# Kernel tuning notes

Measured on AMD Instinct MI355X. Metric: run time of the kernel, lower is better.

Reference implementation:

```python
import jax, jax.numpy as jnp
import numpy as np

B, CIN, COUT, K = 8, 16, 32, 3
D = H = W = 64
NUM_W = CIN * COUT * K ** 3  # 13824
NUM_P = NUM_W + COUT         # 13856


def setup_inputs() -> dict:
    key = jax.random.key(0)
    ks = jax.random.split(key, 10)
    stdv = 1.0 / np.sqrt(CIN * K ** 3)
    return {
        "x": jax.random.normal(ks[0], (B, CIN, D, H, W), jnp.float32),
        "features": jax.random.normal(ks[1], (B, 10), jnp.float32),
        "fc0_w": jax.random.normal(ks[2], (16, 10), jnp.float32) * 0.3,
        "fc0_b": jax.random.normal(ks[3], (16,), jnp.float32) * 0.1,
        "a0": jnp.full((1,), 0.25, jnp.float32),
        "fc1_w": jax.random.normal(ks[4], (8, 16), jnp.float32) * 0.25,
        "fc1_b": jax.random.normal(ks[5], (8,), jnp.float32) * 0.1,
        "a1": jnp.full((1,), 0.25, jnp.float32),
        "wg_w": jax.random.uniform(ks[6], (NUM_P, 8), jnp.float32, -stdv, stdv),
        "wg_b": jax.random.uniform(ks[7], (NUM_P,), jnp.float32, -stdv / 100, stdv / 100),
    }


def _prelu(x, a):
    return jnp.where(x >= 0, x, a * x)


def reference(x, features, fc0_w, fc0_b, a0, fc1_w, fc1_b, a1, wg_w, wg_b):
    # hypernet MLP: [B,10] -> [B,16] -> [B,8] -> [B,NUM_P]
    h = _prelu(features @ fc0_w.T + fc0_b, a0)
    h = _prelu(h @ fc1_w.T + fc1_b, a1)
    params = h @ wg_w.T + wg_b  # [B, NUM_P]
    weights = params[:, :NUM_W].reshape(B, COUT, CIN, K, K, K)
    biases = params[:, NUM_W:]  # [B, COUT]

    def conv_one(xi, wi, bi):
        # xi: [CIN,D,H,W], wi: [COUT,CIN,K,K,K], bi: [COUT]
        y = jax.lax.conv_general_dilated(
            xi[None], wi, window_strides=(1, 1, 1),
            padding=[(1, 1)] * 3,
            dimension_numbers=("NCDHW", "OIDHW", "NCDHW"))
        return y[0] + bi[:, None, None, None]

    return jax.vmap(conv_one)(x, weights, biases)  # [B,COUT,D,H,W]
```

## Files before the change

### kernel.cpp

```cpp
#include <hip/hip_runtime.h>

typedef short short8 __attribute__((ext_vector_type(8)));
typedef float floatx4 __attribute__((ext_vector_type(4)));

#define BB   8
#define CIN  16
#define COUT 32
#define DD   64
#define NUM_W (CIN * COUT * 27)
#define NUM_P (NUM_W + COUT)
#define KPAD  448


__device__ __forceinline__ short f2bf(float f) {
    union { float f; unsigned u; } v; v.f = f;
    unsigned r = v.u + 0x7FFF + ((v.u >> 16) & 1);
    return (short)(r >> 16);
}

__device__ __forceinline__ unsigned pack2bf(float lo, float hi) {
    union { float f; unsigned u; } a, b; a.f = lo; b.f = hi;
    unsigned ra = a.u + 0x7FFF + ((a.u >> 16) & 1);
    unsigned rb = b.u + 0x7FFF + ((b.u >> 16) & 1);
    return (ra >> 16) | (rb & 0xFFFF0000u);
}

__device__ __forceinline__ int swz(int byte) {
    return byte ^ (((byte >> 7) & 7) << 4);
}

__global__ void hyper_kernel(const float* __restrict__ features,
                             const float* __restrict__ fc0_w,
                             const float* __restrict__ fc0_b,
                             const float* __restrict__ a0,
                             const float* __restrict__ fc1_w,
                             const float* __restrict__ fc1_b,
                             const float* __restrict__ a1,
                             const float* __restrict__ wg_w,
                             const float* __restrict__ wg_b,
                             float* __restrict__ h1out,
                             float* __restrict__ biasout) {
    __shared__ float h0[8][16];
    __shared__ float h1s[8][8];
    const int t = threadIdx.x;
    if (t < 128) {
        const int b = t >> 4, i = t & 15;
        float s = fc0_b[i];
        #pragma unroll
        for (int j = 0; j < 10; ++j) s += features[b * 10 + j] * fc0_w[i * 10 + j];
        const float a = a0[0];
        h0[b][i] = (s >= 0.f) ? s : a * s;
    }
    __syncthreads();
    if (t < 64) {
        const int b = t >> 3, i = t & 7;
        float s = fc1_b[i];
        #pragma unroll
        for (int j = 0; j < 16; ++j) s += h0[b][j] * fc1_w[i * 16 + j];
        const float a = a1[0];
        const float r = (s >= 0.f) ? s : a * s;
        h1s[b][i] = r;
        h1out[b * 8 + i] = r;
    }
    __syncthreads();
    {
        const int b = t >> 5, co = t & 31;
        const int p = NUM_W + co;
        float s = wg_b[p];
        #pragma unroll
        for (int j = 0; j < 8; ++j) s += h1s[b][j] * wg_w[p * 8 + j];
        biasout[b * 32 + co] = s;
    }
}

__global__ void wgen_kernel(const float* __restrict__ h1,
                            const float* __restrict__ wg_w,
                            const float* __restrict__ wg_b,
                            short* __restrict__ A) {
    const int b  = blockIdx.y;
    const int id = blockIdx.x * 256 + threadIdx.x;
    const int tap  = id % 28;
    const int rest = id / 28;
    const int ci   = rest & 15;
    const int co   = rest >> 4;
    float val = 0.f;
    if (tap < 27) {
        const int p = co * 432 + ci * 27 + tap;
        float s = wg_b[p];
        #pragma unroll
        for (int j = 0; j < 8; ++j) s += h1[b * 8 + j] * wg_w[p * 8 + j];
        val = s;
    }
    A[(b * 32 + co) * KPAD + tap * 16 + ci] = f2bf(val);
}

__global__ __launch_bounds__(256, 2) void conv_mfma_kernel(
        const float* __restrict__ x,
        const short* __restrict__ A,
        const float* __restrict__ bias,
        float* __restrict__ out) {
    __shared__ uint4 xs4[2376];
    __shared__ uint4 als4[1664];
    char* xsb = (char*)xs4;
    char* alb = (char*)als4;

    const int t    = threadIdx.x;
    const int lane = t & 63;
    const int wave = t >> 6;
    const int n16  = lane & 15;
    const int q    = lane >> 4;

    const int lin = (blockIdx.z * 64 + blockIdx.y) * 16 + blockIdx.x;
    const int o   = (lin & 7) * 1024 + (lin >> 3);
    const int h0  = (o & 15) * 4;
    const int d   = (o >> 4) & 63;
    const int b   = o >> 10;

    const short* Ab = A + (size_t)(b * 32) * KPAD;

    #pragma unroll
    for (int i = 0; i < 7; ++i) {
        const int u = t + i * 256;
        if (u < 1664) {
            const int cm = u >> 6;
            const int c  = cm >> 1, mt = cm & 1;
            const int nn = (u >> 2) & 15, qs = u & 3;
            als4[u] = *(const uint4*)(Ab + (mt * 16 + nn) * KPAD + c * 32 + qs * 8);
        }
    }

    short8 af13[2];
    af13[0] = *(const short8*)(Ab + n16 * KPAD + 13 * 32 + q * 8);
    af13[1] = *(const short8*)(Ab + (16 + n16) * KPAD + 13 * 32 + q * 8);

    if (t < 72) {
        const int rowl = t >> 2;
        const int wz   = ((t >> 1) & 1) * 65;
        const int half = t & 1;
        const uint4 z4 = {0u, 0u, 0u, 0u};
        *(uint4*)(xsb + swz((rowl * 66 + wz) * 32 + half * 16)) = z4;
    }

    const float bv0 = bias[b * 32 + n16];
    const float bv1 = bias[b * 32 + 16 + n16];

    const int tid16 = wave * 4 + q;
    const int cp    = tid16 & 7;
    const int rhalf = tid16 >> 3;
    const int w4    = n16 * 4;
    #pragma unroll
    for (int i = 0; i < 9; ++i) {
        const int rowl = rhalf * 9 + i;
        const int dz = rowl / 6, hz = rowl % 6;
        const int zd = d + dz - 1;
        const int zh = h0 + hz - 1;
        float4 v0 = {0.f, 0.f, 0.f, 0.f};
        float4 v1 = {0.f, 0.f, 0.f, 0.f};
        if (zd >= 0 && zd < DD && zh >= 0 && zh < DD) {
            const size_t gbase =
                (((size_t)(b * CIN + 2 * cp) * DD + zd) * DD + zh) * DD + w4;
            v0 = *(const float4*)(x + gbase);
            v1 = *(const float4*)(x + gbase + (size_t)DD * DD * DD);
        }
        const int rb = (rowl * 66 + (w4 + 1)) * 32 + 4 * cp;
        *(unsigned*)(xsb + swz(rb))      = pack2bf(v0.x, v1.x);
        *(unsigned*)(xsb + swz(rb + 32)) = pack2bf(v0.y, v1.y);
        *(unsigned*)(xsb + swz(rb + 64)) = pack2bf(v0.z, v1.z);
        *(unsigned*)(xsb + swz(rb + 96)) = pack2bf(v0.w, v1.w);
    }
    __syncthreads();

    floatx4 acc[2][4];
    #pragma unroll
    for (int mt = 0; mt < 2; ++mt)
        #pragma unroll
        for (int nt = 0; nt < 4; ++nt) acc[mt][nt] = (floatx4){0.f, 0.f, 0.f, 0.f};

    const int ci_base2 = (q & 1) * 16;
    const int qh       = q >> 1;
    const int aoff     = n16 * 64 + q * 16;
    #pragma unroll
    for (int c = 0; c < 14; ++c) {
        int tap = 2 * c + qh;
        if (tap > 26) tap = 26;
        const int kd = tap / 9;
        const int r  = tap - kd * 9;
        const int kh = r / 3;
        const int kw = r - kh * 3;
        const int rowb = ((kd * 6 + wave + kh) * 66 + kw) * 32 + ci_base2;
        const short8 a0 = (c < 13) ? *(const short8*)(alb + (c * 2) * 1024 + aoff)
                                   : af13[0];
        const short8 a1 = (c < 13) ? *(const short8*)(alb + (c * 2 + 1) * 1024 + aoff)
                                   : af13[1];
        #pragma unroll
        for (int nt = 0; nt < 4; ++nt) {
            const short8 xf = *(const short8*)(xsb + swz(rowb + (nt * 16 + n16) * 32));
            acc[0][nt] = __builtin_amdgcn_mfma_f32_16x16x32_bf16(
                             xf, a0, acc[0][nt], 0, 0, 0);
            acc[1][nt] = __builtin_amdgcn_mfma_f32_16x16x32_bf16(
                             xf, a1, acc[1][nt], 0, 0, 0);
        }
    }

    const int hh = h0 + wave;
    #pragma unroll
    for (int mt = 0; mt < 2; ++mt) {
        const float bv = mt ? bv1 : bv0;
        #pragma unroll
        for (int nt = 0; nt < 4; ++nt) {
            floatx4 rr = acc[mt][nt];
            rr[0] += bv; rr[1] += bv; rr[2] += bv; rr[3] += bv;
            *(floatx4*)(out + (((size_t)(b * COUT + mt * 16 + n16) * DD + d) * DD + hh) * DD
                             + nt * 16 + q * 4) = rr;
        }
    }
}

extern "C" void kernel_launch(void* const* d_in, const int* in_sizes, int n_in,
                              void* d_out, int out_size, void* d_ws, size_t ws_size,
                              hipStream_t stream) {
    const float* x        = (const float*)d_in[0];
    const float* features = (const float*)d_in[1];
    const float* fc0_w    = (const float*)d_in[2];
    const float* fc0_b    = (const float*)d_in[3];
    const float* a0       = (const float*)d_in[4];
    const float* fc1_w    = (const float*)d_in[5];
    const float* fc1_b    = (const float*)d_in[6];
    const float* a1       = (const float*)d_in[7];
    const float* wg_w     = (const float*)d_in[8];
    const float* wg_b     = (const float*)d_in[9];

    float* ws    = (float*)d_ws;
    float* h1    = ws;
    float* biasp = ws + 64;
    short* A     = (short*)(ws + 320);

    hyper_kernel<<<1, 256, 0, stream>>>(features, fc0_w, fc0_b, a0,
                                        fc1_w, fc1_b, a1, wg_w, wg_b, h1, biasp);
    wgen_kernel<<<dim3(56, BB), 256, 0, stream>>>(h1, wg_w, wg_b, A);
    conv_mfma_kernel<<<dim3(16, DD, BB), 256, 0, stream>>>(x, A, biasp, (float*)d_out);
}
```

Baseline: 486.4 us.

## Persist conv blocks over 8 h-tiles with a rolling 6-row halo ring buffer

Each conv block now walks 32 consecutive output rows in 8 iterations instead of handling one 4-row tile. The x slab in shared memory becomes a circular buffer over h, so after the first iteration only the 4 new rows per depth slice are loaded and converted, not all 6. This removes redundant halo reloads and the repeated weight staging per block. The trade-offs are a 16x smaller grid (1024 blocks), an extra barrier per iteration, and serialized load/compute inside each block. s_setprio is also raised around the MFMA loop.

```diff
diff --git a/kernel.cpp b/kernel.cpp
--- a/kernel.cpp
+++ b/kernel.cpp
@@ -94,6 +94,24 @@
     A[(b * 32 + co) * KPAD + tap * 16 + ci] = f2bf(val);
 }
 
+__device__ __forceinline__ void stage_one(const float* __restrict__ x, char* xsb,
+                                          int b, int cp, int w4,
+                                          int dz, int phys, int zd, int zh) {
+    float4 v0 = {0.f, 0.f, 0.f, 0.f};
+    float4 v1 = {0.f, 0.f, 0.f, 0.f};
+    if (zd >= 0 && zd < DD && zh >= 0 && zh < DD) {
+        const size_t gbase =
+            (((size_t)(b * CIN + 2 * cp) * DD + zd) * DD + zh) * DD + w4;
+        v0 = *(const float4*)(x + gbase);
+        v1 = *(const float4*)(x + gbase + (size_t)DD * DD * DD);
+    }
+    const int rb = ((dz * 6 + phys) * 66 + (w4 + 1)) * 32 + 4 * cp;
+    *(unsigned*)(xsb + swz(rb))      = pack2bf(v0.x, v1.x);
+    *(unsigned*)(xsb + swz(rb + 32)) = pack2bf(v0.y, v1.y);
+    *(unsigned*)(xsb + swz(rb + 64)) = pack2bf(v0.z, v1.z);
+    *(unsigned*)(xsb + swz(rb + 96)) = pack2bf(v0.w, v1.w);
+}
+
 __global__ __launch_bounds__(256, 2) void conv_mfma_kernel(
         const float* __restrict__ x,
         const short* __restrict__ A,
@@ -110,11 +128,12 @@
     const int n16  = lane & 15;
     const int q    = lane >> 4;
 
-    const int lin = (blockIdx.z * 64 + blockIdx.y) * 16 + blockIdx.x;
-    const int o   = (lin & 7) * 1024 + (lin >> 3);
-    const int h0  = (o & 15) * 4;
-    const int d   = (o >> 4) & 63;
-    const int b   = o >> 10;
+    const int lin   = blockIdx.x;
+    const int o     = (lin & 7) * 128 + (lin >> 3);
+    const int b     = o >> 7;
+    const int rest  = o & 127;
+    const int d     = rest >> 1;
+    const int hbase = (rest & 1) * 32;
 
     const short* Ab = A + (size_t)(b * 32) * KPAD;
 
@@ -148,70 +167,80 @@
     const int cp    = tid16 & 7;
     const int rhalf = tid16 >> 3;
     const int w4    = n16 * 4;
-    #pragma unroll
-    for (int i = 0; i < 9; ++i) {
-        const int rowl = rhalf * 9 + i;
-        const int dz = rowl / 6, hz = rowl % 6;
-        const int zd = d + dz - 1;
-        const int zh = h0 + hz - 1;
-        float4 v0 = {0.f, 0.f, 0.f, 0.f};
-        float4 v1 = {0.f, 0.f, 0.f, 0.f};
-        if (zd >= 0 && zd < DD && zh >= 0 && zh < DD) {
-            const size_t gbase =
-                (((size_t)(b * CIN + 2 * cp) * DD + zd) * DD + zh) * DD + w4;
-            v0 = *(const float4*)(x + gbase);
-            v1 = *(const float4*)(x + gbase + (size_t)DD * DD * DD);
-        }
-        const int rb = (rowl * 66 + (w4 + 1)) * 32 + 4 * cp;
-        *(unsigned*)(xsb + swz(rb))      = pack2bf(v0.x, v1.x);
-        *(unsigned*)(xsb + swz(rb + 32)) = pack2bf(v0.y, v1.y);
-        *(unsigned*)(xsb + swz(rb + 64)) = pack2bf(v0.z, v1.z);
-        *(unsigned*)(xsb + swz(rb + 96)) = pack2bf(v0.w, v1.w);
-    }
-    __syncthreads();
-
-    floatx4 acc[2][4];
-    #pragma unroll
-    for (int mt = 0; mt < 2; ++mt)
-        #pragma unroll
-        for (int nt = 0; nt < 4; ++nt) acc[mt][nt] = (floatx4){0.f, 0.f, 0.f, 0.f};
 
     const int ci_base2 = (q & 1) * 16;
     const int qh       = q >> 1;
     const int aoff     = n16 * 64 + q * 16;
-    #pragma unroll
-    for (int c = 0; c < 14; ++c) {
-        int tap = 2 * c + qh;
-        if (tap > 26) tap = 26;
-        const int kd = tap / 9;
-        const int r  = tap - kd * 9;
-        const int kh = r / 3;
-        const int kw = r - kh * 3;
-        const int rowb = ((kd * 6 + wave + kh) * 66 + kw) * 32 + ci_base2;
-        const short8 a0 = (c < 13) ? *(const short8*)(alb + (c * 2) * 1024 + aoff)
-                                   : af13[0];
-        const short8 a1 = (c < 13) ? *(const short8*)(alb + (c * 2 + 1) * 1024 + aoff)
-                                   : af13[1];
-        #pragma unroll
-        for (int nt = 0; nt < 4; ++nt) {
-            const short8 xf = *(const short8*)(xsb + swz(rowb + (nt * 16 + n16) * 32));
-            acc[0][nt] = __builtin_amdgcn_mfma_f32_16x16x32_bf16(
-                             xf, a0, acc[0][nt], 0, 0, 0);
-            acc[1][nt] = __builtin_amdgcn_mfma_f32_16x16x32_bf16(
-                             xf, a1, acc[1][nt], 0, 0, 0);
-        }
-    }
-
-    const int hh = h0 + wave;
-    #pragma unroll
-    for (int mt = 0; mt < 2; ++mt) {
-        const float bv = mt ? bv1 : bv0;
-        #pragma unroll
-        for (int nt = 0; nt < 4; ++nt) {
-            floatx4 rr = acc[mt][nt];
-            rr[0] += bv; rr[1] += bv; rr[2] += bv; rr[3] += bv;
-            *(floatx4*)(out + (((size_t)(b * COUT + mt * 16 + n16) * DD + d) * DD + hh) * DD
-                             + nt * 16 + q * 4) = rr;
+
+    #pragma unroll 1
+    for (int it = 0; it < 8; ++it) {
+        const int h0 = hbase + it * 4;
+        const int p  = h0 % 6;
+
+        __syncthreads();
+
+        if (it == 0) {
+            #pragma unroll
+            for (int i = 0; i < 9; ++i) {
+                const int rowl = rhalf * 9 + i;
+                const int dz = rowl / 6, hz = rowl % 6;
+                int phys = p + hz; if (phys >= 6) phys -= 6;
+                stage_one(x, xsb, b, cp, w4, dz, phys, d + dz - 1, h0 + hz - 1);
+            }
+        } else {
+            #pragma unroll
+            for (int i = 0; i < 6; ++i) {
+                const int idx = rhalf * 6 + i;
+                const int dz = idx >> 2, j = idx & 3;
+                int phys = p + 2 + j; if (phys >= 6) phys -= 6;
+                stage_one(x, xsb, b, cp, w4, dz, phys, d + dz - 1, h0 + 1 + j);
+            }
+        }
+        __syncthreads();
+
+        floatx4 acc[2][4];
+        #pragma unroll
+        for (int mt = 0; mt < 2; ++mt)
+            #pragma unroll
+            for (int nt = 0; nt < 4; ++nt) acc[mt][nt] = (floatx4){0.f, 0.f, 0.f, 0.f};
+
+        __builtin_amdgcn_s_setprio(1);
+        #pragma unroll
+        for (int c = 0; c < 14; ++c) {
+            int tap = 2 * c + qh;
+            if (tap > 26) tap = 26;
+            const int kd = tap / 9;
+            const int r  = tap - kd * 9;
+            const int kh = r / 3;
+            const int kw = r - kh * 3;
+            int prow = p + wave + kh; if (prow >= 6) prow -= 6;
+            const int rowb = ((kd * 6 + prow) * 66 + kw) * 32 + ci_base2;
+            const short8 a0 = (c < 13) ? *(const short8*)(alb + (c * 2) * 1024 + aoff)
+                                       : af13[0];
+            const short8 a1 = (c < 13) ? *(const short8*)(alb + (c * 2 + 1) * 1024 + aoff)
+                                       : af13[1];
+            #pragma unroll
+            for (int nt = 0; nt < 4; ++nt) {
+                const short8 xf = *(const short8*)(xsb + swz(rowb + (nt * 16 + n16) * 32));
+                acc[0][nt] = __builtin_amdgcn_mfma_f32_16x16x32_bf16(
+                                 xf, a0, acc[0][nt], 0, 0, 0);
+                acc[1][nt] = __builtin_amdgcn_mfma_f32_16x16x32_bf16(
+                                 xf, a1, acc[1][nt], 0, 0, 0);
+            }
+        }
+        __builtin_amdgcn_s_setprio(0);
+
+        const int hh = h0 + wave;
+        #pragma unroll
+        for (int mt = 0; mt < 2; ++mt) {
+            const float bv = mt ? bv1 : bv0;
+            #pragma unroll
+            for (int nt = 0; nt < 4; ++nt) {
+                floatx4 rr = acc[mt][nt];
+                rr[0] += bv; rr[1] += bv; rr[2] += bv; rr[3] += bv;
+                *(floatx4*)(out + (((size_t)(b * COUT + mt * 16 + n16) * DD + d) * DD + hh) * DD
+                                 + nt * 16 + q * 4) = rr;
+            }
         }
     }
 }
@@ -238,5 +267,5 @@
     hyper_kernel<<<1, 256, 0, stream>>>(features, fc0_w, fc0_b, a0,
                                         fc1_w, fc1_b, a1, wg_w, wg_b, h1, biasp);
     wgen_kernel<<<dim3(56, BB), 256, 0, stream>>>(h1, wg_w, wg_b, A);
-    conv_mfma_kernel<<<dim3(16, DD, BB), 256, 0, stream>>>(x, A, biasp, (float*)d_out);
-}
+    conv_mfma_kernel<<<dim3(1024), 256, 0, stream>>>(x, A, biasp, (float*)d_out);
+}
```

New measurement: 456.8 us. 1.06x faster.
